# Kernel tuning notes

Measured on AMD Instinct MI355X. Metric: run time of the kernel, lower is better.

## Reference

```python
import jax, jax.numpy as jnp
import numpy as np

N_NODES = 100000
N_EDGES = 1600000
D_IN = 256
D_OUT = 256


def _init_linear(key, out_f, in_f):
    # torch nn.Linear default: U(-1/sqrt(in_f), 1/sqrt(in_f))
    kw, kb = jax.random.split(key)
    bound = 1.0 / np.sqrt(in_f)
    W = jax.random.uniform(kw, (out_f, in_f), jnp.float32, -bound, bound)
    b = jax.random.uniform(kb, (out_f,), jnp.float32, -bound, bound)
    return W, b


def setup_inputs() -> dict:
    key = jax.random.key(0)
    ks = jax.random.split(key, 7)
    x = jax.random.normal(ks[0], (N_NODES, D_IN), jnp.float32)
    edge_index = jax.random.randint(ks[1], (2, N_EDGES), 0, N_NODES, jnp.int64)
    W1, b1 = _init_linear(ks[2], D_OUT, D_IN)
    W2, b2 = _init_linear(ks[3], D_OUT // 2, D_OUT)
    W3, b3 = _init_linear(ks[4], D_OUT // 2, D_OUT)
    Wd1, bd1 = _init_linear(ks[5], D_OUT, D_OUT)
    Wd2, bd2 = _init_linear(ks[6], 1, D_OUT)
    return {"x": x, "edge_index": edge_index,
            "W1": W1, "b1": b1, "W2": W2, "b2": b2, "W3": W3, "b3": b3,
            "Wd1": Wd1, "bd1": bd1, "Wd2": Wd2, "bd2": bd2}


def _l2norm(x):
    return x / jnp.linalg.norm(x, axis=-1, keepdims=True)


def reference(x, edge_index, W1, b1, W2, b2, W3, b3, Wd1, bd1, Wd2, bd2):
    src, dst = edge_index[0], edge_index[1]  # source_to_target flow
    x = jax.nn.relu(x @ W1.T + b1)           # [N, D_OUT]
    x = _l2norm(x)
    for _ in range(2):
        # sum-aggregate neighbor messages: scatter-add x[src] into dst
        nm = jax.ops.segment_sum(x[src], dst, num_segments=N_NODES)  # [N, D_OUT]
        x = jax.nn.relu(jnp.concatenate([x @ W2.T + b2, nm @ W3.T + b3], axis=-1))
        x = _l2norm(x)
    x = jax.nn.relu(x @ Wd1.T + bd1)
    return x @ Wd2.T + bd2                    # [N, 1]
```

## Files before the change

kernel.cpp:

```cpp
#include <hip/hip_runtime.h>
#include <math.h>


typedef _Float16 f16x8 __attribute__((ext_vector_type(8)));
typedef float    f32x16 __attribute__((ext_vector_type(16)));

constexpr int DIM = 256;
constexpr int BM  = 128;
constexpr int BK  = 32;
constexpr int SA  = 40;
constexpr int SW  = 40;

__device__ __forceinline__ unsigned pk_hi2(float a, float b) {
    unsigned short ha = __builtin_bit_cast(unsigned short, (_Float16)a);
    unsigned short hb = __builtin_bit_cast(unsigned short, (_Float16)b);
    return (unsigned)ha | ((unsigned)hb << 16);
}
__device__ __forceinline__ unsigned pk_lo2(float a, float b) {
    _Float16 ha = (_Float16)a, hb = (_Float16)b;
    unsigned short la = __builtin_bit_cast(unsigned short, (_Float16)(a - (float)ha));
    unsigned short lb = __builtin_bit_cast(unsigned short, (_Float16)(b - (float)hb));
    return (unsigned)la | ((unsigned)lb << 16);
}
__device__ __forceinline__ unsigned pack_pair(float v) {
    _Float16 hi = (_Float16)v;
    _Float16 lo = (_Float16)(v - (float)hi);
    return (unsigned)__builtin_bit_cast(unsigned short, hi)
         | ((unsigned)__builtin_bit_cast(unsigned short, lo) << 16);
}

template <int AMODE, int EPI>
__device__ __forceinline__
void gemm_body(const void* __restrict__ Av,
               const float* __restrict__ WA, const float* __restrict__ WB,
               const float* __restrict__ bA, const float* __restrict__ bB,
               void* __restrict__ outv,
               const float* __restrict__ wd2, const float* __restrict__ bd2,
               float* __restrict__ out1, int M)
{
    __shared__ __align__(16) _Float16 smem[30720];
    _Float16* As_hi = smem;
    _Float16* As_lo = smem + 5120;
    _Float16* Ws_hi = smem + 10240;
    _Float16* Ws_lo = smem + 20480;

    const int tid  = threadIdx.x;
    const int lane = tid & 63;
    const int w    = tid >> 6;
    const int rh   = w >> 1;
    const int ch   = w & 1;
    const int l31  = lane & 31;
    const int lh   = lane >> 5;
    const int bm0  = blockIdx.x * BM;

    const unsigned* Au = (const unsigned*)Av;
    const int srow = tid >> 3;
    const int sch  = (tid & 7) * 4;

    uint4  pa[4];
    float4 pw[8];

    auto fetchA = [&](int t) {
        const int k0 = t * BK;
        #pragma unroll
        for (int i = 0; i < 4; ++i) {
            const int gr = bm0 + srow + 32 * i;
            uint4 v = {0u, 0u, 0u, 0u};
            if (gr < M) v = *(const uint4*)&Au[(size_t)gr * 256 + k0 + sch];
            pa[i] = v;
        }
    };
    auto fetchW = [&](int t) {
        const int k0 = t * BK;
        #pragma unroll
        for (int i = 0; i < 8; ++i) {
            const int r = srow + 32 * i;
            const float* src = (r < 128) ? &WA[(size_t)r * 256]
                                         : &WB[(size_t)(r - 128) * 256];
            pw[i] = *(const float4*)&src[k0 + sch];
        }
    };
    auto stageA = [&]() {
        #pragma unroll
        for (int i = 0; i < 4; ++i) {
            const int r = srow + 32 * i;
            unsigned h0, h1, l0, l1;
            if (AMODE == 0) {
                const float x0 = __builtin_bit_cast(float, pa[i].x);
                const float x1 = __builtin_bit_cast(float, pa[i].y);
                const float x2 = __builtin_bit_cast(float, pa[i].z);
                const float x3 = __builtin_bit_cast(float, pa[i].w);
                h0 = pk_hi2(x0, x1); h1 = pk_hi2(x2, x3);
                l0 = pk_lo2(x0, x1); l1 = pk_lo2(x2, x3);
            } else {
                h0 = __builtin_amdgcn_perm(pa[i].y, pa[i].x, 0x05040100u);
                l0 = __builtin_amdgcn_perm(pa[i].y, pa[i].x, 0x07060302u);
                h1 = __builtin_amdgcn_perm(pa[i].w, pa[i].z, 0x05040100u);
                l1 = __builtin_amdgcn_perm(pa[i].w, pa[i].z, 0x07060302u);
            }
            uint2 th; th.x = h0; th.y = h1;
            uint2 tl; tl.x = l0; tl.y = l1;
            *(uint2*)&As_hi[r * SA + sch] = th;
            *(uint2*)&As_lo[r * SA + sch] = tl;
        }
    };
    auto stageW = [&]() {
        #pragma unroll
        for (int i = 0; i < 8; ++i) {
            const int r = srow + 32 * i;
            uint2 th; th.x = pk_hi2(pw[i].x, pw[i].y); th.y = pk_hi2(pw[i].z, pw[i].w);
            uint2 tl; tl.x = pk_lo2(pw[i].x, pw[i].y); tl.y = pk_lo2(pw[i].z, pw[i].w);
            *(uint2*)&Ws_hi[r * SW + sch] = th;
            *(uint2*)&Ws_lo[r * SW + sch] = tl;
        }
    };

    f32x16 acc[2][4];
    #pragma unroll
    for (int tr = 0; tr < 2; ++tr)
        #pragma unroll
        for (int tc = 0; tc < 4; ++tc)
            #pragma unroll
            for (int i = 0; i < 16; ++i) acc[tr][tc][i] = 0.0f;

    fetchA(0); fetchW(0);

    #pragma unroll 1
    for (int t = 0; t < DIM / BK; ++t) {
        stageA(); stageW();
        __syncthreads();
        if (t < DIM / BK - 1) { fetchA(t + 1); fetchW(t + 1); }

        #pragma unroll
        for (int ks = 0; ks < 2; ++ks) {
            f16x8 ah[2], al[2], wh[4], wl[4];
            #pragma unroll
            for (int tr = 0; tr < 2; ++tr) {
                const int off = (rh * 64 + tr * 32 + l31) * SA + ks * 16 + lh * 8;
                ah[tr] = *(const f16x8*)&As_hi[off];
                al[tr] = *(const f16x8*)&As_lo[off];
            }
            #pragma unroll
            for (int tc = 0; tc < 4; ++tc) {
                const int off = (ch * 128 + tc * 32 + l31) * SW + ks * 16 + lh * 8;
                wh[tc] = *(const f16x8*)&Ws_hi[off];
                wl[tc] = *(const f16x8*)&Ws_lo[off];
            }
            #pragma unroll
            for (int tr = 0; tr < 2; ++tr)
                #pragma unroll
                for (int tc = 0; tc < 4; ++tc) {
                    acc[tr][tc] = __builtin_amdgcn_mfma_f32_32x32x16_f16(ah[tr], wh[tc], acc[tr][tc], 0, 0, 0);
                    acc[tr][tc] = __builtin_amdgcn_mfma_f32_32x32x16_f16(ah[tr], wl[tc], acc[tr][tc], 0, 0, 0);
                    acc[tr][tc] = __builtin_amdgcn_mfma_f32_32x32x16_f16(al[tr], wh[tc], acc[tr][tc], 0, 0, 0);
                }
        }
        __syncthreads();
    }


    if (EPI == 0) {
        float* z = (float*)outv;
        #pragma unroll
        for (int tr = 0; tr < 2; ++tr)
            #pragma unroll
            for (int i = 0; i < 16; ++i) {
                const int r  = rh * 64 + tr * 32 + 4 * lh + (i & 3) + 8 * (i >> 2);
                const int gr = bm0 + r;
                if (gr < M) {
                    #pragma unroll
                    for (int tc = 0; tc < 4; ++tc)
                        z[(size_t)gr * 256 + ch * 128 + tc * 32 + l31] = acc[tr][tc][i];
                }
            }
        return;
    }

    {
        float bias[4];
        #pragma unroll
        for (int tc = 0; tc < 4; ++tc)
            bias[tc] = (ch ? bB : bA)[tc * 32 + l31];
        #pragma unroll
        for (int tr = 0; tr < 2; ++tr)
            #pragma unroll
            for (int tc = 0; tc < 4; ++tc)
                #pragma unroll
                for (int i = 0; i < 16; ++i)
                    acc[tr][tc][i] = fmaxf(acc[tr][tc][i] + bias[tc], 0.0f);
    }

    float* red = (float*)smem;

    if (EPI == 1) {
        float ss[2][16];
        #pragma unroll
        for (int tr = 0; tr < 2; ++tr)
            #pragma unroll
            for (int i = 0; i < 16; ++i) {
                float s = 0.f;
                #pragma unroll
                for (int tc = 0; tc < 4; ++tc) s += acc[tr][tc][i] * acc[tr][tc][i];
                #pragma unroll
                for (int m = 1; m < 32; m <<= 1) s += __shfl_xor(s, m);
                ss[tr][i] = s;
            }
        const int j  = l31;
        const int ji = j & 15, jt = j >> 4;
        red[ch * 128 + rh * 64 + jt * 32 + 4 * lh + (ji & 3) + 8 * (ji >> 2)] = ss[jt][ji];
        __syncthreads();

        unsigned* hp = (unsigned*)outv;
        #pragma unroll
        for (int tr = 0; tr < 2; ++tr)
            #pragma unroll
            for (int i = 0; i < 16; ++i) {
                const int rl = rh * 64 + tr * 32 + 4 * lh + (i & 3) + 8 * (i >> 2);
                const float inv = 1.0f / sqrtf(red[rl] + red[128 + rl]);
                const int gr = bm0 + rl;
                if (gr < M) {
                    #pragma unroll
                    for (int tc = 0; tc < 4; ++tc)
                        hp[(size_t)gr * 256 + ch * 128 + tc * 32 + l31] =
                            pack_pair(acc[tr][tc][i] * inv);
                }
            }
        return;
    }

    {
        float wv[4];
        #pragma unroll
        for (int tc = 0; tc < 4; ++tc) wv[tc] = wd2[ch * 128 + tc * 32 + l31];
        float dd[2][16];
        #pragma unroll
        for (int tr = 0; tr < 2; ++tr)
            #pragma unroll
            for (int i = 0; i < 16; ++i) {
                float s = 0.f;
                #pragma unroll
                for (int tc = 0; tc < 4; ++tc) s += acc[tr][tc][i] * wv[tc];
                #pragma unroll
                for (int m = 1; m < 32; m <<= 1) s += __shfl_xor(s, m);
                dd[tr][i] = s;
            }
        const int j  = l31;
        const int ji = j & 15, jt = j >> 4;
        red[ch * 128 + rh * 64 + jt * 32 + 4 * lh + (ji & 3) + 8 * (ji >> 2)] = dd[jt][ji];
        __syncthreads();
        if (tid < 128) {
            const int gr = bm0 + tid;
            if (gr < M) out1[gr] = red[tid] + red[128 + tid] + bd2[0];
        }
    }
}

__global__ __launch_bounds__(256, 2)
void gemm_l1(const void* __restrict__ Av,
             const float* __restrict__ WA, const float* __restrict__ WB,
             const float* __restrict__ bA, const float* __restrict__ bB,
             void* __restrict__ outv, int M, int gb,
             const int* __restrict__ ei, int E, int* __restrict__ cnt)
{
    if ((int)blockIdx.x < gb) {
        gemm_body<0, 1>(Av, WA, WB, bA, bB, outv, nullptr, nullptr, nullptr, M);
    } else {
        const int base = ((int)blockIdx.x - gb) * 1024 + threadIdx.x;
        #pragma unroll
        for (int k = 0; k < 4; ++k) {
            const int e = base + k * 256;
            if (e < E) atomicAdd(&cnt[ei[E + e]], 1);
        }
    }
}

template <int DO_FILL>
__global__ __launch_bounds__(256, 2)
void gemm_z(const void* __restrict__ Av,
            const float* __restrict__ WA, const float* __restrict__ WB,
            void* __restrict__ outv, int M, int gb,
            const int* __restrict__ ei, int E,
            int* __restrict__ cursor, int* __restrict__ esrc)
{
    if ((int)blockIdx.x < gb) {
        gemm_body<1, 0>(Av, WA, WB, nullptr, nullptr, outv, nullptr, nullptr, nullptr, M);
    } else if (DO_FILL) {
        const int base = ((int)blockIdx.x - gb) * 1024 + threadIdx.x;
        #pragma unroll
        for (int k = 0; k < 4; ++k) {
            const int e = base + k * 256;
            if (e < E) {
                int d = ei[E + e];
                int p = atomicAdd(&cursor[d], 1);
                esrc[p] = ei[e];
            }
        }
    }
}

__global__ __launch_bounds__(256, 2)
void gemm_head(const void* __restrict__ Av,
               const float* __restrict__ WA, const float* __restrict__ WB,
               const float* __restrict__ bA, const float* __restrict__ bB,
               const float* __restrict__ wd2, const float* __restrict__ bd2,
               float* __restrict__ out1, int M)
{
    gemm_body<1, 2>(Av, WA, WB, bA, bB, nullptr, wd2, bd2, out1, M);
}


__global__ void scan1_kernel(const int* __restrict__ cnt, int n,
                             int* __restrict__ rp, int* __restrict__ sums)
{
    __shared__ int sm[1024];
    const int tid = threadIdx.x;
    const int i = blockIdx.x * 1024 + tid;
    const int v = (i < n) ? cnt[i] : 0;
    sm[tid] = v;
    __syncthreads();
    for (int off = 1; off < 1024; off <<= 1) {
        int t = (tid >= off) ? sm[tid - off] : 0;
        __syncthreads();
        sm[tid] += t;
        __syncthreads();
    }
    if (i < n) rp[i] = sm[tid] - v;
    if (tid == 1023) sums[blockIdx.x] = sm[tid];
}

__global__ void scan2_kernel(int* __restrict__ sums, int n)
{
    __shared__ int sm[128];
    const int tid = threadIdx.x;
    const int v = (tid < n) ? sums[tid] : 0;
    sm[tid] = v;
    __syncthreads();
    for (int off = 1; off < 128; off <<= 1) {
        int t = (tid >= off) ? sm[tid - off] : 0;
        __syncthreads();
        sm[tid] += t;
        __syncthreads();
    }
    if (tid < n) sums[tid] = sm[tid] - v;
}

__global__ void scan3_kernel(int* __restrict__ rp, const int* __restrict__ sums,
                             int* __restrict__ cursor, int n, int E)
{
    int i = blockIdx.x * blockDim.x + threadIdx.x;
    if (i < n) {
        int v = rp[i] + sums[i >> 10];
        rp[i] = v;
        cursor[i] = v;
    }
    if (i == 0) rp[n] = E;
}

__global__ __launch_bounds__(256)
void fin_kernel(const float* __restrict__ z, const int* __restrict__ rp,
                const int* __restrict__ esrc,
                const float* __restrict__ b2, const float* __restrict__ b3,
                unsigned* __restrict__ hp, int M)
{
    const int v    = blockIdx.x * 4 + (threadIdx.x >> 6);
    const int lane = threadIdx.x & 63;
    if (v >= M) return;
    const int beg = rp[v], end = rp[v + 1];
    const int deg = end - beg;

    const float2 z1 = *(const float2*)&z[(size_t)v * DIM + lane * 2];
    const float2 c2 = *(const float2*)&b2[lane * 2];
    const float2 c3 = *(const float2*)&b3[lane * 2];

    const float* z2 = z + 128;
    float ax0 = 0.f, ay0 = 0.f, ax1 = 0.f, ay1 = 0.f;
    float ax2 = 0.f, ay2 = 0.f, ax3 = 0.f, ay3 = 0.f;

    for (int base = 0; base < deg; base += 64) {
        const int cnt = min(64, deg - base);
        int myidx = 0;
        if (lane < cnt) myidx = esrc[beg + base + lane];
        int j = 0;
        for (; j + 3 < cnt; j += 4) {
            const int s0 = __builtin_amdgcn_readlane(myidx, j);
            const int s1 = __builtin_amdgcn_readlane(myidx, j + 1);
            const int s2 = __builtin_amdgcn_readlane(myidx, j + 2);
            const int s3 = __builtin_amdgcn_readlane(myidx, j + 3);
            const float2 g0 = *(const float2*)&z2[(size_t)s0 * DIM + lane * 2];
            const float2 g1 = *(const float2*)&z2[(size_t)s1 * DIM + lane * 2];
            const float2 g2 = *(const float2*)&z2[(size_t)s2 * DIM + lane * 2];
            const float2 g3 = *(const float2*)&z2[(size_t)s3 * DIM + lane * 2];
            ax0 += g0.x; ay0 += g0.y;
            ax1 += g1.x; ay1 += g1.y;
            ax2 += g2.x; ay2 += g2.y;
            ax3 += g3.x; ay3 += g3.y;
        }
        for (; j < cnt; ++j) {
            const int s0 = __builtin_amdgcn_readlane(myidx, j);
            const float2 g0 = *(const float2*)&z2[(size_t)s0 * DIM + lane * 2];
            ax0 += g0.x; ay0 += g0.y;
        }
    }
    const float sx = (ax0 + ax1) + (ax2 + ax3);
    const float sy = (ay0 + ay1) + (ay2 + ay3);

    const float u1x = fmaxf(z1.x + c2.x, 0.f), u1y = fmaxf(z1.y + c2.y, 0.f);
    const float u2x = fmaxf(sx + c3.x, 0.f),  u2y = fmaxf(sy + c3.y, 0.f);

    float ss = u1x * u1x + u1y * u1y + u2x * u2x + u2y * u2y;
    #pragma unroll
    for (int off = 32; off > 0; off >>= 1) ss += __shfl_xor(ss, off);
    const float inv = 1.0f / sqrtf(ss);

    uint2 p1; p1.x = pack_pair(u1x * inv); p1.y = pack_pair(u1y * inv);
    uint2 p2; p2.x = pack_pair(u2x * inv); p2.y = pack_pair(u2y * inv);
    *(uint2*)&hp[(size_t)v * DIM + lane * 2]       = p1;
    *(uint2*)&hp[(size_t)v * DIM + 128 + lane * 2] = p2;
}


extern "C" void kernel_launch(void* const* d_in, const int* in_sizes, int n_in,
                              void* d_out, int out_size, void* d_ws, size_t ws_size,
                              hipStream_t stream)
{
    const float* x   = (const float*)d_in[0];
    const int*   ei  = (const int*)d_in[1];
    const float* W1  = (const float*)d_in[2];
    const float* b1  = (const float*)d_in[3];
    const float* W2  = (const float*)d_in[4];
    const float* b2  = (const float*)d_in[5];
    const float* W3  = (const float*)d_in[6];
    const float* b3  = (const float*)d_in[7];
    const float* Wd1 = (const float*)d_in[8];
    const float* bd1 = (const float*)d_in[9];
    const float* Wd2 = (const float*)d_in[10];
    const float* bd2 = (const float*)d_in[11];
    float* out = (float*)d_out;

    const int M = in_sizes[0] / DIM;
    const int E = in_sizes[1] / 2;

    unsigned* hp  = (unsigned*)d_ws;
    float*    z   = (float*)(hp + (size_t)M * DIM);
    int*   rp     = (int*)(z + (size_t)M * DIM);
    int*   cursor = rp + (M + 1);
    int*   esrc   = cursor + M;
    int*   sums   = esrc + E;

    hipMemsetAsync(cursor, 0, sizeof(int) * M, stream);

    const int gb  = (M + BM - 1) / BM;
    const int hb  = (E + 1023) / 1024;
    const int nb1 = (M + 1023) / 1024;
    const int fb  = (M + 3) / 4;

    gemm_l1<<<gb + hb, 256, 0, stream>>>(
        x, W1, W1 + 128 * DIM, b1, b1 + 128, hp, M, gb, ei, E, cursor);

    scan1_kernel<<<nb1, 1024, 0, stream>>>(cursor, M, rp, sums);
    scan2_kernel<<<1, 128, 0, stream>>>(sums, nb1);
    scan3_kernel<<<(M + 255) / 256, 256, 0, stream>>>(rp, sums, cursor, M, E);

    gemm_z<1><<<gb + hb, 256, 0, stream>>>(hp, W2, W3, z, M, gb, ei, E, cursor, esrc);
    fin_kernel<<<fb, 256, 0, stream>>>(z, rp, esrc, b2, b3, hp, M);

    gemm_z<0><<<gb, 256, 0, stream>>>(hp, W2, W3, z, M, gb, nullptr, 0, nullptr, nullptr);
    fin_kernel<<<fb, 256, 0, stream>>>(z, rp, esrc, b2, b3, hp, M);

    gemm_head<<<gb, 256, 0, stream>>>(
        hp, Wd1, Wd1 + 128 * DIM, bd1, bd1 + 128, Wd2, bd2, out, M);
}
```

Measured before the change: 768.1 us.

## Prepack weights into MFMA fragment layout and stream GEMM operands from registers

Adds a kernel that converts the three weight matrices once per call into hi/lo fp16 pairs already arranged in MFMA fragment order. The GEMM body drops shared-memory staging and block-wide barriers. Each wave now loads its A rows and prepacked W fragments straight from global memory into registers, double-buffered across k-steps. The row tile shrinks to 64 and occupancy rises to 3 blocks per SM. This removes the per-block fp32-to-fp16 split of the weights and the LDS traffic. In exchange, each wave re-reads the weight fragments from global memory or cache, and there is one extra kernel launch.

```diff
diff --git a/kernel.cpp b/kernel.cpp
--- a/kernel.cpp
+++ b/kernel.cpp
@@ -6,22 +6,8 @@
 typedef float    f32x16 __attribute__((ext_vector_type(16)));
 
 constexpr int DIM = 256;
-constexpr int BM  = 128;
-constexpr int BK  = 32;
-constexpr int SA  = 40;
-constexpr int SW  = 40;
-
-__device__ __forceinline__ unsigned pk_hi2(float a, float b) {
-    unsigned short ha = __builtin_bit_cast(unsigned short, (_Float16)a);
-    unsigned short hb = __builtin_bit_cast(unsigned short, (_Float16)b);
-    return (unsigned)ha | ((unsigned)hb << 16);
-}
-__device__ __forceinline__ unsigned pk_lo2(float a, float b) {
-    _Float16 ha = (_Float16)a, hb = (_Float16)b;
-    unsigned short la = __builtin_bit_cast(unsigned short, (_Float16)(a - (float)ha));
-    unsigned short lb = __builtin_bit_cast(unsigned short, (_Float16)(b - (float)hb));
-    return (unsigned)la | ((unsigned)lb << 16);
-}
+constexpr int BM  = 64;
+
 __device__ __forceinline__ unsigned pack_pair(float v) {
     _Float16 hi = (_Float16)v;
     _Float16 lo = (_Float16)(v - (float)hi);
@@ -29,150 +15,149 @@
          | ((unsigned)__builtin_bit_cast(unsigned short, lo) << 16);
 }
 
+__global__ __launch_bounds__(256)
+void pack_w_kernel(const float* __restrict__ WA0, const float* __restrict__ WB0,
+                   const float* __restrict__ WA1, const float* __restrict__ WB1,
+                   const float* __restrict__ WA2, const float* __restrict__ WB2,
+                   _Float16* __restrict__ d0, _Float16* __restrict__ d1,
+                   _Float16* __restrict__ d2)
+{
+    const int layer = (int)blockIdx.x >> 6;
+    const int tid   = ((int)blockIdx.x & 63) * 256 + threadIdx.x;
+    const float* WA = layer == 0 ? WA0 : layer == 1 ? WA1 : WA2;
+    const float* WB = layer == 0 ? WB0 : layer == 1 ? WB1 : WB2;
+    _Float16* dst   = layer == 0 ? d0  : layer == 1 ? d1  : d2;
+
+    const int lane = tid & 63;
+    const int frag = tid >> 6;
+    const int nt = frag & 7;
+    const int ks = (frag >> 3) & 1;
+    const int t  = (frag >> 4) & 7;
+    const int hl = frag >> 7;
+    const int n  = nt * 32 + (lane & 31);
+    const int k0 = t * 32 + ks * 16 + (lane >> 5) * 8;
+    const float* src = (n < 128) ? &WA[(size_t)n * 256] : &WB[(size_t)(n - 128) * 256];
+
+    f16x8 o;
+    #pragma unroll
+    for (int j = 0; j < 8; ++j) {
+        const float v = src[k0 + j];
+        const _Float16 h = (_Float16)v;
+        o[j] = hl ? (_Float16)(v - (float)h) : h;
+    }
+    *(f16x8*)&dst[(size_t)tid * 8] = o;
+}
+
 template <int AMODE, int EPI>
 __device__ __forceinline__
-void gemm_body(const void* __restrict__ Av,
-               const float* __restrict__ WA, const float* __restrict__ WB,
-               const float* __restrict__ bA, const float* __restrict__ bB,
-               void* __restrict__ outv,
-               const float* __restrict__ wd2, const float* __restrict__ bd2,
-               float* __restrict__ out1, int M)
-{
-    __shared__ __align__(16) _Float16 smem[30720];
-    _Float16* As_hi = smem;
-    _Float16* As_lo = smem + 5120;
-    _Float16* Ws_hi = smem + 10240;
-    _Float16* Ws_lo = smem + 20480;
-
+void gemm2_body(const void* __restrict__ Av, const _Float16* __restrict__ Wpk,
+                const float* __restrict__ bA, const float* __restrict__ bB,
+                void* __restrict__ outv,
+                const float* __restrict__ wd2, const float* __restrict__ bd2,
+                float* __restrict__ out1, int M)
+{
     const int tid  = threadIdx.x;
     const int lane = tid & 63;
     const int w    = tid >> 6;
-    const int rh   = w >> 1;
-    const int ch   = w & 1;
+    const int wr   = w >> 1;
+    const int wc   = w & 1;
     const int l31  = lane & 31;
     const int lh   = lane >> 5;
-    const int bm0  = blockIdx.x * BM;
-
-    const unsigned* Au = (const unsigned*)Av;
-    const int srow = tid >> 3;
-    const int sch  = (tid & 7) * 4;
-
-    uint4  pa[4];
-    float4 pw[8];
-
-    auto fetchA = [&](int t) {
-        const int k0 = t * BK;
-        #pragma unroll
-        for (int i = 0; i < 4; ++i) {
-            const int gr = bm0 + srow + 32 * i;
-            uint4 v = {0u, 0u, 0u, 0u};
-            if (gr < M) v = *(const uint4*)&Au[(size_t)gr * 256 + k0 + sch];
-            pa[i] = v;
-        }
+    const int bm0  = (int)blockIdx.x * BM;
+
+    const int arow = bm0 + wr * 32 + l31;
+    const int ar   = arow < M ? arow : (M - 1);
+
+    const char* a_p = (const char*)Av + (size_t)ar * 1024 + lh * 32;
+
+    const char* wh_p = (const char*)Wpk + (size_t)(wc * 4 * 64 + lane) * 16;
+    const char* wl_p = wh_p + 128 * 64 * 16;
+
+    f32x16 acc[4];
+    #pragma unroll
+    for (int tc = 0; tc < 4; ++tc)
+        #pragma unroll
+        for (int i = 0; i < 16; ++i) acc[tc][i] = 0.0f;
+
+    uint4 A0[2], A1[2];
+    f16x8 W0[4], W1[4], wl[4];
+
+    auto PA = [&](int s, uint4* A) {
+        A[0] = *(const uint4*)(a_p + s * 64);
+        A[1] = *(const uint4*)(a_p + s * 64 + 16);
     };
-    auto fetchW = [&](int t) {
-        const int k0 = t * BK;
-        #pragma unroll
-        for (int i = 0; i < 8; ++i) {
-            const int r = srow + 32 * i;
-            const float* src = (r < 128) ? &WA[(size_t)r * 256]
-                                         : &WB[(size_t)(r - 128) * 256];
-            pw[i] = *(const float4*)&src[k0 + sch];
-        }
+    auto PWH = [&](int s, f16x8* W) {
+        #pragma unroll
+        for (int tc = 0; tc < 4; ++tc)
+            W[tc] = *(const f16x8*)(wh_p + s * 8192 + tc * 1024);
     };
-    auto stageA = [&]() {
-        #pragma unroll
-        for (int i = 0; i < 4; ++i) {
-            const int r = srow + 32 * i;
-            unsigned h0, h1, l0, l1;
-            if (AMODE == 0) {
-                const float x0 = __builtin_bit_cast(float, pa[i].x);
-                const float x1 = __builtin_bit_cast(float, pa[i].y);
-                const float x2 = __builtin_bit_cast(float, pa[i].z);
-                const float x3 = __builtin_bit_cast(float, pa[i].w);
-                h0 = pk_hi2(x0, x1); h1 = pk_hi2(x2, x3);
-                l0 = pk_lo2(x0, x1); l1 = pk_lo2(x2, x3);
-            } else {
-                h0 = __builtin_amdgcn_perm(pa[i].y, pa[i].x, 0x05040100u);
-                l0 = __builtin_amdgcn_perm(pa[i].y, pa[i].x, 0x07060302u);
-                h1 = __builtin_amdgcn_perm(pa[i].w, pa[i].z, 0x05040100u);
-                l1 = __builtin_amdgcn_perm(pa[i].w, pa[i].z, 0x07060302u);
+    auto WL = [&](int s) {
+        #pragma unroll
+        for (int tc = 0; tc < 4; ++tc)
+            wl[tc] = *(const f16x8*)(wl_p + s * 8192 + tc * 1024);
+    };
+    auto COMP = [&](const uint4* A, const f16x8* W) {
+        f16x8 ah, al;
+        if constexpr (AMODE == 1) {
+            uint4 uh, ul;
+            uh.x = __builtin_amdgcn_perm(A[0].y, A[0].x, 0x05040100u);
+            uh.y = __builtin_amdgcn_perm(A[0].w, A[0].z, 0x05040100u);
+            uh.z = __builtin_amdgcn_perm(A[1].y, A[1].x, 0x05040100u);
+            uh.w = __builtin_amdgcn_perm(A[1].w, A[1].z, 0x05040100u);
+            ul.x = __builtin_amdgcn_perm(A[0].y, A[0].x, 0x07060302u);
+            ul.y = __builtin_amdgcn_perm(A[0].w, A[0].z, 0x07060302u);
+            ul.z = __builtin_amdgcn_perm(A[1].y, A[1].x, 0x07060302u);
+            ul.w = __builtin_amdgcn_perm(A[1].w, A[1].z, 0x07060302u);
+            ah = __builtin_bit_cast(f16x8, uh);
+            al = __builtin_bit_cast(f16x8, ul);
+        } else {
+            const float fv[8] = {
+                __builtin_bit_cast(float, A[0].x), __builtin_bit_cast(float, A[0].y),
+                __builtin_bit_cast(float, A[0].z), __builtin_bit_cast(float, A[0].w),
+                __builtin_bit_cast(float, A[1].x), __builtin_bit_cast(float, A[1].y),
+                __builtin_bit_cast(float, A[1].z), __builtin_bit_cast(float, A[1].w)};
+            #pragma unroll
+            for (int j = 0; j < 8; ++j) {
+                const _Float16 h = (_Float16)fv[j];
+                ah[j] = h;
+                al[j] = (_Float16)(fv[j] - (float)h);
             }
-            uint2 th; th.x = h0; th.y = h1;
-            uint2 tl; tl.x = l0; tl.y = l1;
-            *(uint2*)&As_hi[r * SA + sch] = th;
-            *(uint2*)&As_lo[r * SA + sch] = tl;
-        }
+        }
+        #pragma unroll
+        for (int tc = 0; tc < 4; ++tc)
+            acc[tc] = __builtin_amdgcn_mfma_f32_32x32x16_f16(ah, W[tc], acc[tc], 0, 0, 0);
+        #pragma unroll
+        for (int tc = 0; tc < 4; ++tc)
+            acc[tc] = __builtin_amdgcn_mfma_f32_32x32x16_f16(ah, wl[tc], acc[tc], 0, 0, 0);
+        #pragma unroll
+        for (int tc = 0; tc < 4; ++tc)
+            acc[tc] = __builtin_amdgcn_mfma_f32_32x32x16_f16(al, W[tc], acc[tc], 0, 0, 0);
     };
-    auto stageW = [&]() {
-        #pragma unroll
-        for (int i = 0; i < 8; ++i) {
-            const int r = srow + 32 * i;
-            uint2 th; th.x = pk_hi2(pw[i].x, pw[i].y); th.y = pk_hi2(pw[i].z, pw[i].w);
-            uint2 tl; tl.x = pk_lo2(pw[i].x, pw[i].y); tl.y = pk_lo2(pw[i].z, pw[i].w);
-            *(uint2*)&Ws_hi[r * SW + sch] = th;
-            *(uint2*)&Ws_lo[r * SW + sch] = tl;
-        }
-    };
-
-    f32x16 acc[2][4];
-    #pragma unroll
-    for (int tr = 0; tr < 2; ++tr)
-        #pragma unroll
-        for (int tc = 0; tc < 4; ++tc)
-            #pragma unroll
-            for (int i = 0; i < 16; ++i) acc[tr][tc][i] = 0.0f;
-
-    fetchA(0); fetchW(0);
-
+
+    PA(0, A0); PWH(0, W0);
     #pragma unroll 1
-    for (int t = 0; t < DIM / BK; ++t) {
-        stageA(); stageW();
-        __syncthreads();
-        if (t < DIM / BK - 1) { fetchA(t + 1); fetchW(t + 1); }
-
-        #pragma unroll
-        for (int ks = 0; ks < 2; ++ks) {
-            f16x8 ah[2], al[2], wh[4], wl[4];
-            #pragma unroll
-            for (int tr = 0; tr < 2; ++tr) {
-                const int off = (rh * 64 + tr * 32 + l31) * SA + ks * 16 + lh * 8;
-                ah[tr] = *(const f16x8*)&As_hi[off];
-                al[tr] = *(const f16x8*)&As_lo[off];
+    for (int s = 0; s < 16; s += 2) {
+        WL(s);
+        PA(s + 1, A1); PWH(s + 1, W1);
+        COMP(A0, W0);
+        WL(s + 1);
+        if (s + 2 < 16) { PA(s + 2, A0); PWH(s + 2, W0); }
+        COMP(A1, W1);
+    }
+
+
+    if constexpr (EPI == 0) {
+        float* zz = (float*)outv;
+        #pragma unroll
+        for (int i = 0; i < 16; ++i) {
+            const int rl = wr * 32 + 4 * lh + (i & 3) + 8 * (i >> 2);
+            const int gr = bm0 + rl;
+            if (gr < M) {
+                #pragma unroll
+                for (int tc = 0; tc < 4; ++tc)
+                    zz[(size_t)gr * 256 + wc * 128 + tc * 32 + l31] = acc[tc][i];
             }
-            #pragma unroll
-            for (int tc = 0; tc < 4; ++tc) {
-                const int off = (ch * 128 + tc * 32 + l31) * SW + ks * 16 + lh * 8;
-                wh[tc] = *(const f16x8*)&Ws_hi[off];
-                wl[tc] = *(const f16x8*)&Ws_lo[off];
-            }
-            #pragma unroll
-            for (int tr = 0; tr < 2; ++tr)
-                #pragma unroll
-                for (int tc = 0; tc < 4; ++tc) {
-                    acc[tr][tc] = __builtin_amdgcn_mfma_f32_32x32x16_f16(ah[tr], wh[tc], acc[tr][tc], 0, 0, 0);
-                    acc[tr][tc] = __builtin_amdgcn_mfma_f32_32x32x16_f16(ah[tr], wl[tc], acc[tr][tc], 0, 0, 0);
-                    acc[tr][tc] = __builtin_amdgcn_mfma_f32_32x32x16_f16(al[tr], wh[tc], acc[tr][tc], 0, 0, 0);
-                }
-        }
-        __syncthreads();
-    }
-
-
-    if (EPI == 0) {
-        float* z = (float*)outv;
-        #pragma unroll
-        for (int tr = 0; tr < 2; ++tr)
-            #pragma unroll
-            for (int i = 0; i < 16; ++i) {
-                const int r  = rh * 64 + tr * 32 + 4 * lh + (i & 3) + 8 * (i >> 2);
-                const int gr = bm0 + r;
-                if (gr < M) {
-                    #pragma unroll
-                    for (int tc = 0; tc < 4; ++tc)
-                        z[(size_t)gr * 256 + ch * 128 + tc * 32 + l31] = acc[tr][tc][i];
-                }
-            }
+        }
         return;
     }
 
@@ -180,90 +165,75 @@
         float bias[4];
         #pragma unroll
         for (int tc = 0; tc < 4; ++tc)
-            bias[tc] = (ch ? bB : bA)[tc * 32 + l31];
-        #pragma unroll
-        for (int tr = 0; tr < 2; ++tr)
-            #pragma unroll
-            for (int tc = 0; tc < 4; ++tc)
+            bias[tc] = (wc ? bB : bA)[tc * 32 + l31];
+        #pragma unroll
+        for (int tc = 0; tc < 4; ++tc)
+            #pragma unroll
+            for (int i = 0; i < 16; ++i)
+                acc[tc][i] = fmaxf(acc[tc][i] + bias[tc], 0.0f);
+    }
+
+    if constexpr (EPI == 1) {
+        __shared__ float red[128];
+        #pragma unroll
+        for (int i = 0; i < 16; ++i) {
+            float s = 0.f;
+            #pragma unroll
+            for (int tc = 0; tc < 4; ++tc) s += acc[tc][i] * acc[tc][i];
+            #pragma unroll
+            for (int m = 1; m < 32; m <<= 1) s += __shfl_xor(s, m);
+            if (l31 == i)
+                red[wc * 64 + wr * 32 + 4 * lh + (i & 3) + 8 * (i >> 2)] = s;
+        }
+        __syncthreads();
+
+        unsigned* hpo = (unsigned*)outv;
+        #pragma unroll
+        for (int i = 0; i < 16; ++i) {
+            const int rl  = wr * 32 + 4 * lh + (i & 3) + 8 * (i >> 2);
+            const float inv = 1.0f / sqrtf(red[rl] + red[64 + rl]);
+            const int gr  = bm0 + rl;
+            if (gr < M) {
                 #pragma unroll
-                for (int i = 0; i < 16; ++i)
-                    acc[tr][tc][i] = fmaxf(acc[tr][tc][i] + bias[tc], 0.0f);
-    }
-
-    float* red = (float*)smem;
-
-    if (EPI == 1) {
-        float ss[2][16];
-        #pragma unroll
-        for (int tr = 0; tr < 2; ++tr)
-            #pragma unroll
-            for (int i = 0; i < 16; ++i) {
-                float s = 0.f;
-                #pragma unroll
-                for (int tc = 0; tc < 4; ++tc) s += acc[tr][tc][i] * acc[tr][tc][i];
-                #pragma unroll
-                for (int m = 1; m < 32; m <<= 1) s += __shfl_xor(s, m);
-                ss[tr][i] = s;
+                for (int tc = 0; tc < 4; ++tc)
+                    hpo[(size_t)gr * 256 + wc * 128 + tc * 32 + l31] =
+                        pack_pair(acc[tc][i] * inv);
             }
-        const int j  = l31;
-        const int ji = j & 15, jt = j >> 4;
-        red[ch * 128 + rh * 64 + jt * 32 + 4 * lh + (ji & 3) + 8 * (ji >> 2)] = ss[jt][ji];
-        __syncthreads();
-
-        unsigned* hp = (unsigned*)outv;
-        #pragma unroll
-        for (int tr = 0; tr < 2; ++tr)
-            #pragma unroll
-            for (int i = 0; i < 16; ++i) {
-                const int rl = rh * 64 + tr * 32 + 4 * lh + (i & 3) + 8 * (i >> 2);
-                const float inv = 1.0f / sqrtf(red[rl] + red[128 + rl]);
-                const int gr = bm0 + rl;
-                if (gr < M) {
-                    #pragma unroll
-                    for (int tc = 0; tc < 4; ++tc)
-                        hp[(size_t)gr * 256 + ch * 128 + tc * 32 + l31] =
-                            pack_pair(acc[tr][tc][i] * inv);
-                }
-            }
+        }
         return;
     }
 
-    {
+    if constexpr (EPI == 2) {
+        __shared__ float red[128];
         float wv[4];
         #pragma unroll
-        for (int tc = 0; tc < 4; ++tc) wv[tc] = wd2[ch * 128 + tc * 32 + l31];
-        float dd[2][16];
-        #pragma unroll
-        for (int tr = 0; tr < 2; ++tr)
-            #pragma unroll
-            for (int i = 0; i < 16; ++i) {
-                float s = 0.f;
-                #pragma unroll
-                for (int tc = 0; tc < 4; ++tc) s += acc[tr][tc][i] * wv[tc];
-                #pragma unroll
-                for (int m = 1; m < 32; m <<= 1) s += __shfl_xor(s, m);
-                dd[tr][i] = s;
-            }
-        const int j  = l31;
-        const int ji = j & 15, jt = j >> 4;
-        red[ch * 128 + rh * 64 + jt * 32 + 4 * lh + (ji & 3) + 8 * (ji >> 2)] = dd[jt][ji];
-        __syncthreads();
-        if (tid < 128) {
+        for (int tc = 0; tc < 4; ++tc) wv[tc] = wd2[wc * 128 + tc * 32 + l31];
+        #pragma unroll
+        for (int i = 0; i < 16; ++i) {
+            float s = 0.f;
+            #pragma unroll
+            for (int tc = 0; tc < 4; ++tc) s += acc[tc][i] * wv[tc];
+            #pragma unroll
+            for (int m = 1; m < 32; m <<= 1) s += __shfl_xor(s, m);
+            if (l31 == i)
+                red[wc * 64 + wr * 32 + 4 * lh + (i & 3) + 8 * (i >> 2)] = s;
+        }
+        __syncthreads();
+        if (tid < 64) {
             const int gr = bm0 + tid;
-            if (gr < M) out1[gr] = red[tid] + red[128 + tid] + bd2[0];
-        }
-    }
-}
-
-__global__ __launch_bounds__(256, 2)
-void gemm_l1(const void* __restrict__ Av,
-             const float* __restrict__ WA, const float* __restrict__ WB,
+            if (gr < M) out1[gr] = red[tid] + red[64 + tid] + bd2[0];
+        }
+    }
+}
+
+__global__ __launch_bounds__(256, 3)
+void gemm_l1(const float* __restrict__ x, const _Float16* __restrict__ wpk,
              const float* __restrict__ bA, const float* __restrict__ bB,
-             void* __restrict__ outv, int M, int gb,
+             unsigned* __restrict__ hp, int M, int gb,
              const int* __restrict__ ei, int E, int* __restrict__ cnt)
 {
     if ((int)blockIdx.x < gb) {
-        gemm_body<0, 1>(Av, WA, WB, bA, bB, outv, nullptr, nullptr, nullptr, M);
+        gemm2_body<0, 1>(x, wpk, bA, bB, hp, nullptr, nullptr, nullptr, M);
     } else {
         const int base = ((int)blockIdx.x - gb) * 1024 + threadIdx.x;
         #pragma unroll
@@ -275,15 +245,14 @@
 }
 
 template <int DO_FILL>
-__global__ __launch_bounds__(256, 2)
-void gemm_z(const void* __restrict__ Av,
-            const float* __restrict__ WA, const float* __restrict__ WB,
-            void* __restrict__ outv, int M, int gb,
+__global__ __launch_bounds__(256, 3)
+void gemm_z(const void* __restrict__ Av, const _Float16* __restrict__ wpk,
+            float* __restrict__ z, int M, int gb,
             const int* __restrict__ ei, int E,
             int* __restrict__ cursor, int* __restrict__ esrc)
 {
     if ((int)blockIdx.x < gb) {
-        gemm_body<1, 0>(Av, WA, WB, nullptr, nullptr, outv, nullptr, nullptr, nullptr, M);
+        gemm2_body<1, 0>(Av, wpk, nullptr, nullptr, z, nullptr, nullptr, nullptr, M);
     } else if (DO_FILL) {
         const int base = ((int)blockIdx.x - gb) * 1024 + threadIdx.x;
         #pragma unroll
@@ -298,14 +267,13 @@
     }
 }
 
-__global__ __launch_bounds__(256, 2)
-void gemm_head(const void* __restrict__ Av,
-               const float* __restrict__ WA, const float* __restrict__ WB,
+__global__ __launch_bounds__(256, 3)
+void gemm_head(const void* __restrict__ Av, const _Float16* __restrict__ wpk,
                const float* __restrict__ bA, const float* __restrict__ bB,
                const float* __restrict__ wd2, const float* __restrict__ bd2,
                float* __restrict__ out1, int M)
 {
-    gemm_body<1, 2>(Av, WA, WB, bA, bB, nullptr, wd2, bd2, out1, M);
+    gemm2_body<1, 2>(Av, wpk, bA, bB, nullptr, wd2, bd2, out1, M);
 }
 
 
@@ -447,7 +415,16 @@
     int*   esrc   = cursor + M;
     int*   sums   = esrc + E;
 
+    size_t woff = (size_t)((char*)(sums + 128) - (char*)d_ws);
+    woff = (woff + 255) & ~(size_t)255;
+    _Float16* wpk1 = (_Float16*)((char*)d_ws + woff);
+    _Float16* wpk2 = wpk1 + 131072;
+    _Float16* wpkd = wpk2 + 131072;
+
     hipMemsetAsync(cursor, 0, sizeof(int) * M, stream);
+
+    pack_w_kernel<<<192, 256, 0, stream>>>(
+        W1, W1 + 128 * DIM, W2, W3, Wd1, Wd1 + 128 * DIM, wpk1, wpk2, wpkd);
 
     const int gb  = (M + BM - 1) / BM;
     const int hb  = (E + 1023) / 1024;
@@ -455,18 +432,18 @@
     const int fb  = (M + 3) / 4;
 
     gemm_l1<<<gb + hb, 256, 0, stream>>>(
-        x, W1, W1 + 128 * DIM, b1, b1 + 128, hp, M, gb, ei, E, cursor);
+        x, wpk1, b1, b1 + 128, hp, M, gb, ei, E, cursor);
 
     scan1_kernel<<<nb1, 1024, 0, stream>>>(cursor, M, rp, sums);
     scan2_kernel<<<1, 128, 0, stream>>>(sums, nb1);
     scan3_kernel<<<(M + 255) / 256, 256, 0, stream>>>(rp, sums, cursor, M, E);
 
-    gemm_z<1><<<gb + hb, 256, 0, stream>>>(hp, W2, W3, z, M, gb, ei, E, cursor, esrc);
+    gemm_z<1><<<gb + hb, 256, 0, stream>>>(hp, wpk2, z, M, gb, ei, E, cursor, esrc);
     fin_kernel<<<fb, 256, 0, stream>>>(z, rp, esrc, b2, b3, hp, M);
 
-    gemm_z<0><<<gb, 256, 0, stream>>>(hp, W2, W3, z, M, gb, nullptr, 0, nullptr, nullptr);
+    gemm_z<0><<<gb, 256, 0, stream>>>(hp, wpk2, z, M, gb, nullptr, 0, nullptr, nullptr);
     fin_kernel<<<fb, 256, 0, stream>>>(z, rp, esrc, b2, b3, hp, M);
 
     gemm_head<<<gb, 256, 0, stream>>>(
-        hp, Wd1, Wd1 + 128 * DIM, bd1, bd1 + 128, Wd2, bd2, out, M);
-}
+        hp, wpkd, bd1, bd1 + 128, Wd2, bd2, out, M);
+}
```

Measured after the change: 844.2 us. +9.9%, slower.

## Build CSR via two-level bucket sort with shared-memory histograms

Applied to the files above, without the earlier changes.

Replaces the per-node global atomic count, three-kernel scan and global-atomic fill with a bucketed counting sort. Edges are first histogrammed into 256-node buckets in shared memory, then scattered as (dst,src) pairs into bucket order inside gemm_l1. A per-bucket kernel then does the local counting sort and writes the row pointers. This cuts contended global atomics and random scatter writes, at the cost of an extra pass over the edges and reusing the z buffer as scratch. NBMAX is hard-coded to 392 buckets, which limits the node count.

```diff
diff --git a/kernel.cpp b/kernel.cpp
--- a/kernel.cpp
+++ b/kernel.cpp
@@ -10,6 +10,7 @@
 constexpr int BK  = 32;
 constexpr int SA  = 40;
 constexpr int SW  = 40;
+constexpr int NBMAX = 392;
 
 __device__ __forceinline__ unsigned pk_hi2(float a, float b) {
     unsigned short ha = __builtin_bit_cast(unsigned short, (_Float16)a);
@@ -260,42 +261,39 @@
              const float* __restrict__ WA, const float* __restrict__ WB,
              const float* __restrict__ bA, const float* __restrict__ bB,
              void* __restrict__ outv, int M, int gb,
-             const int* __restrict__ ei, int E, int* __restrict__ cnt)
+             const int* __restrict__ ei, int E, int nb,
+             int* __restrict__ gcur, int2* __restrict__ ebuf)
 {
     if ((int)blockIdx.x < gb) {
         gemm_body<0, 1>(Av, WA, WB, bA, bB, outv, nullptr, nullptr, nullptr, M);
     } else {
-        const int base = ((int)blockIdx.x - gb) * 1024 + threadIdx.x;
-        #pragma unroll
-        for (int k = 0; k < 4; ++k) {
-            const int e = base + k * 256;
-            if (e < E) atomicAdd(&cnt[ei[E + e]], 1);
-        }
-    }
-}
-
-template <int DO_FILL>
+        __shared__ int h[NBMAX], cur[NBMAX];
+        const int tid = threadIdx.x;
+        const int b   = (int)blockIdx.x - gb;
+        for (int t = tid; t < nb; t += 256) h[t] = 0;
+        __syncthreads();
+        const int EB = (E + 127) >> 7;
+        const int e0 = b * EB, e1 = min(E, e0 + EB);
+        for (int e = e0 + tid; e < e1; e += 256)
+            atomicAdd(&h[ei[E + e] >> 8], 1);
+        __syncthreads();
+        for (int t = tid; t < nb; t += 256)
+            cur[t] = atomicAdd(&gcur[t], h[t]);
+        __syncthreads();
+        for (int e = e0 + tid; e < e1; e += 256) {
+            const int d = ei[E + e];
+            const int p = atomicAdd(&cur[d >> 8], 1);
+            ebuf[p] = make_int2(d, ei[e]);
+        }
+    }
+}
+
 __global__ __launch_bounds__(256, 2)
 void gemm_z(const void* __restrict__ Av,
             const float* __restrict__ WA, const float* __restrict__ WB,
-            void* __restrict__ outv, int M, int gb,
-            const int* __restrict__ ei, int E,
-            int* __restrict__ cursor, int* __restrict__ esrc)
-{
-    if ((int)blockIdx.x < gb) {
-        gemm_body<1, 0>(Av, WA, WB, nullptr, nullptr, outv, nullptr, nullptr, nullptr, M);
-    } else if (DO_FILL) {
-        const int base = ((int)blockIdx.x - gb) * 1024 + threadIdx.x;
-        #pragma unroll
-        for (int k = 0; k < 4; ++k) {
-            const int e = base + k * 256;
-            if (e < E) {
-                int d = ei[E + e];
-                int p = atomicAdd(&cursor[d], 1);
-                esrc[p] = ei[e];
-            }
-        }
-    }
+            void* __restrict__ outv, int M)
+{
+    gemm_body<1, 0>(Av, WA, WB, nullptr, nullptr, outv, nullptr, nullptr, nullptr, M);
 }
 
 __global__ __launch_bounds__(256, 2)
@@ -309,51 +307,79 @@
 }
 
 
-__global__ void scan1_kernel(const int* __restrict__ cnt, int n,
-                             int* __restrict__ rp, int* __restrict__ sums)
-{
-    __shared__ int sm[1024];
+__global__ __launch_bounds__(256)
+void hist_kernel(const int* __restrict__ ei, int E, int nb,
+                 int* __restrict__ ghist)
+{
+    __shared__ int h[NBMAX];
     const int tid = threadIdx.x;
-    const int i = blockIdx.x * 1024 + tid;
-    const int v = (i < n) ? cnt[i] : 0;
+    for (int t = tid; t < nb; t += 256) h[t] = 0;
+    __syncthreads();
+    const int EB = (E + 127) >> 7;
+    const int e0 = (int)blockIdx.x * EB, e1 = min(E, e0 + EB);
+    for (int e = e0 + tid; e < e1; e += 256)
+        atomicAdd(&h[ei[E + e] >> 8], 1);
+    __syncthreads();
+    for (int t = tid; t < nb; t += 256)
+        if (h[t]) atomicAdd(&ghist[t], h[t]);
+}
+
+__global__ __launch_bounds__(512)
+void scanb_kernel(const int* __restrict__ ghist, int* __restrict__ gboff,
+                  int* __restrict__ gcur, int* __restrict__ rp, int M, int E,
+                  int nb)
+{
+    __shared__ int sm[512];
+    const int tid = threadIdx.x;
+    const int v = (tid < nb) ? ghist[tid] : 0;
     sm[tid] = v;
     __syncthreads();
-    for (int off = 1; off < 1024; off <<= 1) {
+    for (int off = 1; off < 512; off <<= 1) {
         int t = (tid >= off) ? sm[tid - off] : 0;
         __syncthreads();
         sm[tid] += t;
         __syncthreads();
     }
-    if (i < n) rp[i] = sm[tid] - v;
-    if (tid == 1023) sums[blockIdx.x] = sm[tid];
-}
-
-__global__ void scan2_kernel(int* __restrict__ sums, int n)
-{
-    __shared__ int sm[128];
+    if (tid < nb) {
+        const int ex = sm[tid] - v;
+        gboff[tid] = ex;
+        gcur[tid]  = ex;
+    }
+    if (tid == 0) { gboff[nb] = E; rp[M] = E; }
+}
+
+__global__ __launch_bounds__(256)
+void bucket_kernel(const int2* __restrict__ ebuf, const int* __restrict__ gboff,
+                   int* __restrict__ rp, int* __restrict__ esrc, int M)
+{
+    const int b   = (int)blockIdx.x;
     const int tid = threadIdx.x;
-    const int v = (tid < n) ? sums[tid] : 0;
-    sm[tid] = v;
-    __syncthreads();
-    for (int off = 1; off < 128; off <<= 1) {
+    const int base = gboff[b], top = gboff[b + 1];
+    const int d0 = b << 8;
+    __shared__ int c[256], sm[256], cur[256];
+    c[tid] = 0;
+    __syncthreads();
+    for (int j = base + tid; j < top; j += 256)
+        atomicAdd(&c[ebuf[j].x - d0], 1);
+    __syncthreads();
+    sm[tid] = c[tid];
+    __syncthreads();
+    for (int off = 1; off < 256; off <<= 1) {
         int t = (tid >= off) ? sm[tid - off] : 0;
         __syncthreads();
         sm[tid] += t;
         __syncthreads();
     }
-    if (tid < n) sums[tid] = sm[tid] - v;
-}
-
-__global__ void scan3_kernel(int* __restrict__ rp, const int* __restrict__ sums,
-                             int* __restrict__ cursor, int n, int E)
-{
-    int i = blockIdx.x * blockDim.x + threadIdx.x;
-    if (i < n) {
-        int v = rp[i] + sums[i >> 10];
-        rp[i] = v;
-        cursor[i] = v;
-    }
-    if (i == 0) rp[n] = E;
+    const int excl = sm[tid] - c[tid];
+    const int d = d0 + tid;
+    if (d < M) rp[d] = base + excl;
+    cur[tid] = base + excl;
+    __syncthreads();
+    for (int j = base + tid; j < top; j += 256) {
+        const int2 e = ebuf[j];
+        const int p = atomicAdd(&cur[e.x - d0], 1);
+        esrc[p] = e.y;
+    }
 }
 
 __global__ __launch_bounds__(256)
@@ -439,32 +465,34 @@
 
     const int M = in_sizes[0] / DIM;
     const int E = in_sizes[1] / 2;
+    const int nb = (M + 255) >> 8;
 
     unsigned* hp  = (unsigned*)d_ws;
     float*    z   = (float*)(hp + (size_t)M * DIM);
     int*   rp     = (int*)(z + (size_t)M * DIM);
-    int*   cursor = rp + (M + 1);
-    int*   esrc   = cursor + M;
-    int*   sums   = esrc + E;
-
-    hipMemsetAsync(cursor, 0, sizeof(int) * M, stream);
+    int*   esrc   = rp + (M + 1);
+    int*   ghist  = esrc + E;
+    int*   gboff  = ghist + nb;
+    int*   gcur   = gboff + nb + 1;
+    int2*  ebuf   = (int2*)z;
+
+    hipMemsetAsync(ghist, 0, sizeof(int) * nb, stream);
 
     const int gb  = (M + BM - 1) / BM;
-    const int hb  = (E + 1023) / 1024;
-    const int nb1 = (M + 1023) / 1024;
     const int fb  = (M + 3) / 4;
 
-    gemm_l1<<<gb + hb, 256, 0, stream>>>(
-        x, W1, W1 + 128 * DIM, b1, b1 + 128, hp, M, gb, ei, E, cursor);
-
-    scan1_kernel<<<nb1, 1024, 0, stream>>>(cursor, M, rp, sums);
-    scan2_kernel<<<1, 128, 0, stream>>>(sums, nb1);
-    scan3_kernel<<<(M + 255) / 256, 256, 0, stream>>>(rp, sums, cursor, M, E);
-
-    gemm_z<1><<<gb + hb, 256, 0, stream>>>(hp, W2, W3, z, M, gb, ei, E, cursor, esrc);
+    hist_kernel<<<128, 256, 0, stream>>>(ei, E, nb, ghist);
+    scanb_kernel<<<1, 512, 0, stream>>>(ghist, gboff, gcur, rp, M, E, nb);
+
+    gemm_l1<<<gb + 128, 256, 0, stream>>>(
+        x, W1, W1 + 128 * DIM, b1, b1 + 128, hp, M, gb, ei, E, nb, gcur, ebuf);
+
+    bucket_kernel<<<nb, 256, 0, stream>>>(ebuf, gboff, rp, esrc, M);
+
+    gemm_z<<<gb, 256, 0, stream>>>(hp, W2, W3, z, M);
     fin_kernel<<<fb, 256, 0, stream>>>(z, rp, esrc, b2, b3, hp, M);
 
-    gemm_z<0><<<gb, 256, 0, stream>>>(hp, W2, W3, z, M, gb, nullptr, 0, nullptr, nullptr);
+    gemm_z<<<gb, 256, 0, stream>>>(hp, W2, W3, z, M);
     fin_kernel<<<fb, 256, 0, stream>>>(z, rp, esrc, b2, b3, hp, M);
 
     gemm_head<<<gb, 256, 0, stream>>>(
```

Measured after the change: 722.3 us. 6.0% less time.
